# Optimization experiments

Hardware: AMD Instinct MI355X
Metric: run time of the kernel (lower is better)

## Reference

```python
import jax, jax.numpy as jnp
import numpy as np

B, S, D, H, KV = 2, 2048, 1024, 16, 64
NUM_BUCKETS, MAX_DIST = 32, 128
LN_EPS = 1e-6


def _relative_position_bucket(rel_pos, num_buckets=NUM_BUCKETS, max_distance=MAX_DIST):
    # bidirectional (encoder) T5 bucketing
    nb = num_buckets // 2
    rb = (rel_pos > 0).astype(jnp.int32) * nb
    rp = jnp.abs(rel_pos)
    max_exact = nb // 2
    is_small = rp < max_exact
    rp_f = jnp.maximum(rp, 1).astype(jnp.float32)
    large = max_exact + (
        jnp.log(rp_f / max_exact) / np.log(max_distance / max_exact) * (nb - max_exact)
    ).astype(jnp.int32)
    large = jnp.minimum(large, nb - 1)
    return rb + jnp.where(is_small, rp, large)


def _compute_bias(rel_emb, q_len, k_len):
    ctx = jnp.arange(q_len)[:, None]
    mem = jnp.arange(k_len)[None, :]
    buckets = _relative_position_bucket(mem - ctx)            # (q, k)
    bias = rel_emb[buckets]                                   # (q, k, H)
    return jnp.transpose(bias, (2, 0, 1))[None]               # (1, H, q, k)


def setup_inputs() -> dict:
    key = jax.random.key(0)
    ks = jax.random.split(key, 8)
    return {
        "hidden_states": jax.random.normal(ks[0], (B, S, D), jnp.float32),
        "attention_mask": jnp.zeros((B, 1, 1, S), jnp.float32),
        "delete_gate_mask": jax.random.normal(ks[1], (B, S, 1), jnp.float32),
        "wq": jax.random.normal(ks[2], (D, H * KV), jnp.float32) * 0.02,
        "wk": jax.random.normal(ks[3], (D, H * KV), jnp.float32) * 0.02,
        "wv": jax.random.normal(ks[4], (D, H * KV), jnp.float32) * 0.02,
        "wo": jax.random.normal(ks[5], (H * KV, D), jnp.float32) * 0.02,
        "rel_emb": jax.random.normal(ks[6], (NUM_BUCKETS, H), jnp.float32) * 0.5,
        "ln_weight": jnp.ones((D,), jnp.float32),
    }


def reference(hidden_states, attention_mask, delete_gate_mask, wq, wk, wv, wo, rel_emb, ln_weight):
    # T5LayerNorm: RMS norm, no mean subtraction, no bias
    var = jnp.mean(jnp.square(hidden_states), axis=-1, keepdims=True)
    normed = hidden_states * jax.lax.rsqrt(var + LN_EPS) * ln_weight

    # project and split heads: (B, H, S, KV). T5 does NOT scale by 1/sqrt(d).
    q = jnp.einsum('bsd,dhk->bhsk', normed, wq.reshape(D, H, KV))
    k = jnp.einsum('bsd,dhk->bhsk', normed, wk.reshape(D, H, KV))
    v = jnp.einsum('bsd,dhk->bhsk', normed, wv.reshape(D, H, KV))

    scores = jnp.einsum('bhqk,bhmk->bhqm', q, k)              # (B, H, S, S)

    position_bias = _compute_bias(rel_emb, S, S) + attention_mask  # (B, H, S, S) via broadcast
    scores = scores + position_bias
    # delete gate: (B, S, 1) -> additive over key axis
    scores = scores + delete_gate_mask[:, :, 0][:, None, None, :]

    attn = jax.nn.softmax(scores.astype(jnp.float32), axis=-1).astype(scores.dtype)
    ctx = jnp.einsum('bhqm,bhmk->bhqk', attn, v)              # (B, H, S, KV)
    ctx = jnp.transpose(ctx, (0, 2, 1, 3)).reshape(B, S, H * KV)
    attn_out = ctx @ wo                                       # (B, S, D)

    return hidden_states + attn_out
```

## Files before the change

### kernel.cpp

```cpp
#include <hip/hip_runtime.h>
#include <math.h>

#define SQ_LEN 2048
#define NB 2
#define DIM 1024
#define NH 16
#define BS (NB * SQ_LEN)

typedef __attribute__((ext_vector_type(8))) unsigned short ushort8;
typedef __attribute__((ext_vector_type(8))) __bf16 bf16x8;
typedef __attribute__((ext_vector_type(4))) float f32x4;

__device__ __forceinline__ unsigned short f2bfu(float x) {
    __bf16 h = (__bf16)x;
    return __builtin_bit_cast(unsigned short, h);
}
__device__ __forceinline__ bf16x8 ldb8(const unsigned short* p) {
    return __builtin_bit_cast(bf16x8, *(const ushort8*)p);
}
__device__ __forceinline__ void gl16(const unsigned short* g, unsigned short* l) {
    __builtin_amdgcn_global_load_lds(
        (const __attribute__((address_space(1))) unsigned int*)g,
        (__attribute__((address_space(3))) unsigned int*)l, 16, 0, 0);
}
__device__ __forceinline__ int pxor(int row) {
    return (((row & 7) ^ (((row >> 3) & 1) << 1)) << 3);
}
#define MFMA16(a, b, c) __builtin_amdgcn_mfma_f32_16x16x32_bf16(a, b, c, 0, 0, 0)
#define SM_SHIFT 16.0f

__global__ __launch_bounds__(256) void k_bias_table(const float* __restrict__ rel_emb,
                                                    float* __restrict__ table) {
    int i = blockIdx.x * 256 + threadIdx.x;
    int h = i >> 12;
    int idx = i & 4095;
    int rel = idx - 2048;
    int rb = (rel > 0) ? 16 : 0;
    int rp = rel < 0 ? -rel : rel;
    int v;
    if (rp < 8) {
        v = rp;
    } else {
        double lg = log((double)rp / 8.0) / log(16.0) * 8.0;
        int li = (int)lg;
        v = 8 + li;
        if (v > 15) v = 15;
    }
    table[i] = rel_emb[(rb + v) * NH + h] - SM_SHIFT;
}

__global__ __launch_bounds__(256) void k_kvbias(const float* __restrict__ am,
                                                const float* __restrict__ dg,
                                                float* __restrict__ kvb) {
    int i = blockIdx.x * 256 + threadIdx.x;
    kvb[i] = am[i] + dg[i];
}

__global__ __launch_bounds__(256) void k_wconv(const float* __restrict__ w0,
                                               const float* __restrict__ w1,
                                               const float* __restrict__ w2,
                                               const float* __restrict__ w3,
                                               unsigned short* __restrict__ wt) {
    int z = blockIdx.z;
    const float* w = (z == 0) ? w0 : (z == 1) ? w1 : (z == 2) ? w2 : w3;
    unsigned short* o = wt + (size_t)z * DIM * DIM;
    __shared__ float tile[64][68];
    int k0 = blockIdx.x * 64, n0 = blockIdx.y * 64;
    int t = threadIdx.x;
    {
        int r = t & 63, cs = (t >> 6) * 16;
#pragma unroll
        for (int u = 0; u < 4; ++u) {
            float4 v4 = *(const float4*)(w + (size_t)(k0 + r) * DIM + n0 + cs + 4 * u);
            *(float4*)&tile[r][cs + 4 * u] = v4;
        }
    }
    __syncthreads();
    {
        int n = t & 63, ks = (t >> 6) * 16;
        unsigned buf[8];
#pragma unroll
        for (int kk = 0; kk < 8; ++kk) {
            buf[kk] = (unsigned)f2bfu(tile[ks + 2 * kk][n]) |
                      ((unsigned)f2bfu(tile[ks + 2 * kk + 1][n]) << 16);
        }
        unsigned short* op = o + (size_t)(n0 + n) * DIM + k0 + ks;
        *(uint4*)op = make_uint4(buf[0], buf[1], buf[2], buf[3]);
        *(uint4*)(op + 8) = make_uint4(buf[4], buf[5], buf[6], buf[7]);
    }
}

__global__ __launch_bounds__(256) void k_rmsnorm(const float* __restrict__ x,
                                                 const float* __restrict__ w,
                                                 unsigned short* __restrict__ o) {
    int row = blockIdx.x;
    int t = threadIdx.x;
    float4 v = ((const float4*)(x + (size_t)row * DIM))[t];
    float ss = v.x * v.x + v.y * v.y + v.z * v.z + v.w * v.w;
#pragma unroll
    for (int m = 1; m < 64; m <<= 1) ss += __shfl_xor(ss, m);
    __shared__ float wsum[4];
    if ((t & 63) == 0) wsum[t >> 6] = ss;
    __syncthreads();
    float tot = wsum[0] + wsum[1] + wsum[2] + wsum[3];
    float r = rsqrtf(tot * (1.0f / DIM) + 1e-6f);
    float4 wt = ((const float4*)w)[t];
    uint2 pk;
    pk.x = (unsigned)f2bfu(v.x * r * wt.x) | ((unsigned)f2bfu(v.y * r * wt.y) << 16);
    pk.y = (unsigned)f2bfu(v.z * r * wt.z) | ((unsigned)f2bfu(v.w * r * wt.w) << 16);
    *(uint2*)(o + (size_t)row * DIM + t * 4) = pk;
}

__global__ __launch_bounds__(256) void k_gemm_qkv(const unsigned short* __restrict__ A,
                                                  const unsigned short* __restrict__ Wt,
                                                  unsigned short* __restrict__ Qo,
                                                  unsigned short* __restrict__ Ko,
                                                  unsigned short* __restrict__ Vto) {
    __shared__ unsigned short As[128 * 64];
    __shared__ unsigned short Bs[128 * 64];
    int m0 = blockIdx.x * 128;
    int mat = blockIdx.y >> 3;
    int n0 = (blockIdx.y & 7) * 128;
    const unsigned short* Bp = Wt + (size_t)mat * (DIM * DIM);
    int t = threadIdx.x;
    int w = t >> 6, l = t & 63;
    int wm = (w >> 1) * 64, wn = (w & 1) * 64;
    int g = l >> 4, n16 = l & 15;
    int c0 = (g ^ (n16 & 7)) * 8;
    int c1 = ((4 + g) ^ (n16 & 7)) * 8;
    f32x4 acc[4][4];
#pragma unroll
    for (int i = 0; i < 4; ++i)
#pragma unroll
        for (int j = 0; j < 4; ++j) acc[i][j] = 0.0f;

    for (int k0 = 0; k0 < DIM; k0 += 64) {
        __syncthreads();
#pragma unroll
        for (int u = 0; u < 4; ++u) {
            int ci = t + 256 * u;
            int row = ci >> 3;
            int sc = ((ci & 7) ^ (row & 7)) * 8;
            gl16(A + (size_t)(m0 + row) * DIM + k0 + sc, &As[ci * 8]);
            gl16(Bp + (size_t)(n0 + row) * DIM + k0 + sc, &Bs[ci * 8]);
        }
        __syncthreads();
        bf16x8 af[2][4], bf[2][4];
#pragma unroll
        for (int ks = 0; ks < 2; ++ks) {
            int cs = ks ? c1 : c0;
#pragma unroll
            for (int x = 0; x < 4; ++x) {
                af[ks][x] = ldb8(&As[(wm + x * 16 + n16) * 64 + cs]);
                bf[ks][x] = ldb8(&Bs[(wn + x * 16 + n16) * 64 + cs]);
            }
        }
#pragma unroll
        for (int ks = 0; ks < 2; ++ks)
#pragma unroll
            for (int mf = 0; mf < 4; ++mf)
#pragma unroll
                for (int nf = 0; nf < 4; ++nf)
                    acc[mf][nf] = MFMA16(af[ks][mf], bf[ks][nf], acc[mf][nf]);
    }
    if (mat < 2) {
        unsigned short* C = (mat == 0) ? Qo : Ko;
#pragma unroll
        for (int mf = 0; mf < 4; ++mf)
#pragma unroll
            for (int nf = 0; nf < 4; ++nf) {
                size_t base = (size_t)(m0 + wm + mf * 16 + 4 * g) * DIM + (n0 + wn + nf * 16 + n16);
#pragma unroll
                for (int r = 0; r < 4; ++r) C[base + (size_t)r * DIM] = f2bfu(acc[mf][nf][r]);
            }
    } else {
        int b = m0 >> 11;
        int sq = (m0 & 2047) + wm;
#pragma unroll
        for (int mf = 0; mf < 4; ++mf)
#pragma unroll
            for (int nf = 0; nf < 4; ++nf) {
                int n = n0 + wn + nf * 16 + n16;
                int s = sq + mf * 16 + 4 * g;
                uint2 pk;
                pk.x = (unsigned)f2bfu(acc[mf][nf][0]) | ((unsigned)f2bfu(acc[mf][nf][1]) << 16);
                pk.y = (unsigned)f2bfu(acc[mf][nf][2]) | ((unsigned)f2bfu(acc[mf][nf][3]) << 16);
                *(uint2*)(Vto + ((size_t)b << 21) + (size_t)n * SQ_LEN + s) = pk;
            }
    }
}

__global__ __launch_bounds__(256) void k_gemm_out(const unsigned short* __restrict__ A,
                                                  const unsigned short* __restrict__ Bt,
                                                  const float* __restrict__ resid,
                                                  float* __restrict__ Co) {
    __shared__ unsigned short As[128 * 64];
    __shared__ unsigned short Bs[128 * 64];
    int m0 = blockIdx.x * 128;
    int n0 = blockIdx.y * 128;
    int t = threadIdx.x;
    int w = t >> 6, l = t & 63;
    int wm = (w >> 1) * 64, wn = (w & 1) * 64;
    int g = l >> 4, n16 = l & 15;
    int c0 = (g ^ (n16 & 7)) * 8;
    int c1 = ((4 + g) ^ (n16 & 7)) * 8;
    f32x4 acc[4][4];
#pragma unroll
    for (int i = 0; i < 4; ++i)
#pragma unroll
        for (int j = 0; j < 4; ++j) acc[i][j] = 0.0f;

    for (int k0 = 0; k0 < DIM; k0 += 64) {
        __syncthreads();
#pragma unroll
        for (int u = 0; u < 4; ++u) {
            int ci = t + 256 * u;
            int row = ci >> 3;
            int sc = ((ci & 7) ^ (row & 7)) * 8;
            gl16(A + (size_t)(m0 + row) * DIM + k0 + sc, &As[ci * 8]);
            gl16(Bt + (size_t)(n0 + row) * DIM + k0 + sc, &Bs[ci * 8]);
        }
        __syncthreads();
        bf16x8 af[2][4], bf[2][4];
#pragma unroll
        for (int ks = 0; ks < 2; ++ks) {
            int cs = ks ? c1 : c0;
#pragma unroll
            for (int x = 0; x < 4; ++x) {
                af[ks][x] = ldb8(&As[(wm + x * 16 + n16) * 64 + cs]);
                bf[ks][x] = ldb8(&Bs[(wn + x * 16 + n16) * 64 + cs]);
            }
        }
#pragma unroll
        for (int ks = 0; ks < 2; ++ks)
#pragma unroll
            for (int mf = 0; mf < 4; ++mf)
#pragma unroll
                for (int nf = 0; nf < 4; ++nf)
                    acc[mf][nf] = MFMA16(af[ks][mf], bf[ks][nf], acc[mf][nf]);
    }
#pragma unroll
    for (int mf = 0; mf < 4; ++mf)
#pragma unroll
        for (int nf = 0; nf < 4; ++nf) {
            size_t base = (size_t)(m0 + wm + mf * 16 + 4 * g) * DIM + (n0 + wn + nf * 16 + n16);
#pragma unroll
            for (int r = 0; r < 4; ++r) {
                size_t off = base + (size_t)r * DIM;
                Co[off] = acc[mf][nf][r] + resid[off];
            }
        }
}

__global__ __launch_bounds__(256) void k_attn(const unsigned short* __restrict__ Q,
                                              const unsigned short* __restrict__ K,
                                              const unsigned short* __restrict__ Vt,
                                              const float* __restrict__ table,
                                              const float* __restrict__ kvb,
                                              unsigned short* __restrict__ ctx) {
    int qt = blockIdx.x;
    int bh = blockIdx.y;
    int b = bh >> 4, h = bh & 15;
    int qbase = qt * 128;

    __shared__ unsigned short Ks[64 * 64];
    __shared__ unsigned short Vs[64 * 64];
    __shared__ unsigned short Ps[4][32 * 64];
    __shared__ float tabR[4][200];

    int t = threadIdx.x, w = t >> 6, l = t & 63;
    int g = l >> 4, n16 = l & 15;
    int c0 = (g ^ (n16 & 7)) * 8;
    int c1 = ((4 + g) ^ (n16 & 7)) * 8;
    int pxr = pxor(n16);

    const unsigned short* qp = Q + (size_t)(b * SQ_LEN + qbase + 32 * w) * DIM + h * 64;
    const unsigned short* kp = K + (size_t)(b * SQ_LEN) * DIM + h * 64;
    const unsigned short* vp = Vt + ((size_t)b << 21) + (size_t)(h * 64) * SQ_LEN;
    const float* tabh = table + h * 4096;

    bf16x8 aq[2][2];
#pragma unroll
    for (int sub = 0; sub < 2; ++sub)
#pragma unroll
        for (int ks = 0; ks < 2; ++ks)
            aq[sub][ks] = ldb8(qp + (size_t)(sub * 16 + n16) * DIM + ks * 32 + g * 8);

    float sl[2][4] = {};
    f32x4 o[2][4];
#pragma unroll
    for (int sub = 0; sub < 2; ++sub)
#pragma unroll
        for (int f = 0; f < 4; ++f) o[sub][f] = 0.0f;

    int base_i[2];
#pragma unroll
    for (int sub = 0; sub < 2; ++sub)
        base_i[sub] = 130 - 32 * w + n16 - 16 * sub - 4 * g;
    int tb = 1918 - qbase;

    for (int kt = 0; kt < SQ_LEN / 64; ++kt) {
        __syncthreads();
        {
#pragma unroll
            for (int u = 0; u < 2; ++u) {
                int ci = t + 256 * u;
                int row = ci >> 3;
                int sc = ((ci & 7) ^ (row & 7)) * 8;
                gl16(kp + (size_t)(kt * 64 + row) * DIM + sc, &Ks[ci * 8]);
                gl16(vp + (size_t)row * SQ_LEN + kt * 64 + sc, &Vs[ci * 8]);
            }
        }
        {
#pragma unroll
            for (int u = 0; u < 4; ++u) {
                int e = t + 256 * u;
                int m = e >> 8, j = e & 255;
                if (j < 194) {
                    int gi = kt * 64 + tb + j + m;
                    gi = gi < 0 ? 0 : (gi > 4095 ? 4095 : gi);
                    tabR[m][j] = tabh[gi];
                }
            }
        }
        __syncthreads();

        const float* kvbp = kvb + b * SQ_LEN + kt * 64 + n16;
        f32x4 s4[2][4];
#pragma unroll
        for (int sub = 0; sub < 2; ++sub)
#pragma unroll
            for (int f = 0; f < 4; ++f) {
                int s = base_i[sub] + 16 * f - 3;
                int m = s & 3;
                f32x4 tv = *(const f32x4*)&tabR[m][s - m];
                float kb = kvbp[f * 16];
                f32x4 iv;
                iv[0] = tv[3] + kb; iv[1] = tv[2] + kb;
                iv[2] = tv[1] + kb; iv[3] = tv[0] + kb;
                s4[sub][f] = iv;
            }
#pragma unroll
        for (int ks = 0; ks < 2; ++ks) {
            int cs = ks ? c1 : c0;
#pragma unroll
            for (int f = 0; f < 4; ++f) {
                bf16x8 kf = ldb8(&Ks[(f * 16 + n16) * 64 + cs]);
#pragma unroll
                for (int sub = 0; sub < 2; ++sub)
                    s4[sub][f] = MFMA16(aq[sub][ks], kf, s4[sub][f]);
            }
        }
#pragma unroll
        for (int sub = 0; sub < 2; ++sub)
#pragma unroll
            for (int f = 0; f < 4; ++f) {
#pragma unroll
                for (int r = 0; r < 4; ++r) {
                    float p = __expf(s4[sub][f][r]);
                    sl[sub][r] += p;
                    int pr = sub * 16 + 4 * g + r;
                    Ps[w][pr * 64 + ((f * 16 + n16) ^ pxor(pr))] = f2bfu(p);
                }
            }
#pragma unroll
        for (int ks = 0; ks < 2; ++ks) {
            int cs = ks ? c1 : c0;
            int csp = ((ks ? (4 + g) : g) * 8) ^ pxr;
            bf16x8 ap[2];
#pragma unroll
            for (int sub = 0; sub < 2; ++sub)
                ap[sub] = ldb8(&Ps[w][(sub * 16 + n16) * 64 + csp]);
#pragma unroll
            for (int f = 0; f < 4; ++f) {
                bf16x8 vf = ldb8(&Vs[(f * 16 + n16) * 64 + cs]);
#pragma unroll
                for (int sub = 0; sub < 2; ++sub)
                    o[sub][f] = MFMA16(ap[sub], vf, o[sub][f]);
            }
        }
    }
    float inv[2][4];
#pragma unroll
    for (int sub = 0; sub < 2; ++sub)
#pragma unroll
        for (int r = 0; r < 4; ++r) {
            float s = sl[sub][r];
            s += __shfl_xor(s, 1);
            s += __shfl_xor(s, 2);
            s += __shfl_xor(s, 4);
            s += __shfl_xor(s, 8);
            inv[sub][r] = 1.0f / s;
        }
    unsigned short* cp = ctx + (size_t)(b * SQ_LEN + qbase + 32 * w) * DIM + h * 64;
#pragma unroll
    for (int sub = 0; sub < 2; ++sub)
#pragma unroll
        for (int f = 0; f < 4; ++f)
#pragma unroll
            for (int r = 0; r < 4; ++r)
                cp[(size_t)(sub * 16 + 4 * g + r) * DIM + f * 16 + n16] =
                    f2bfu(o[sub][f][r] * inv[sub][r]);
}

extern "C" void kernel_launch(void* const* d_in, const int* in_sizes, int n_in,
                              void* d_out, int out_size, void* d_ws, size_t ws_size,
                              hipStream_t stream) {
    const float* hidden = (const float*)d_in[0];
    const float* amask  = (const float*)d_in[1];
    const float* dg     = (const float*)d_in[2];
    const float* wq     = (const float*)d_in[3];
    const float* wk     = (const float*)d_in[4];
    const float* wv     = (const float*)d_in[5];
    const float* wo     = (const float*)d_in[6];
    const float* rel    = (const float*)d_in[7];
    const float* lnw    = (const float*)d_in[8];
    float* out = (float*)d_out;
    char* ws = (char*)d_ws;

    const size_t MB8 = (size_t)BS * DIM * 2;
    unsigned short* normed = (unsigned short*)(ws);
    unsigned short* qb     = (unsigned short*)(ws + MB8);
    unsigned short* kb     = (unsigned short*)(ws + 2 * MB8);
    unsigned short* vtb    = (unsigned short*)(ws + 3 * MB8);
    unsigned short* ctxb   = (unsigned short*)(ws + 4 * MB8);
    unsigned short* wt     = (unsigned short*)(ws + 5 * MB8);
    float* table           = (float*)(ws + 6 * MB8);
    float* kvb             = (float*)(ws + 6 * MB8 + NH * 4096 * 4);

    k_wconv<<<dim3(16, 16, 4), 256, 0, stream>>>(wq, wk, wv, wo, wt);
    k_bias_table<<<NH * 4096 / 256, 256, 0, stream>>>(rel, table);
    k_kvbias<<<BS / 256, 256, 0, stream>>>(amask, dg, kvb);
    k_rmsnorm<<<BS, 256, 0, stream>>>(hidden, lnw, normed);

    k_gemm_qkv<<<dim3(BS / 128, 24), 256, 0, stream>>>(normed, wt, qb, kb, vtb);
    k_attn<<<dim3(SQ_LEN / 128, NB * NH), 256, 0, stream>>>(qb, kb, vtb, table, kvb, ctxb);
    k_gemm_out<<<dim3(BS / 128, 8), 256, 0, stream>>>(ctxb, wt + 3 * (size_t)DIM * DIM,
                                                      hidden, out);
}
```

Before: 234.1 us.

## Use 8 waves per attention block, smaller out-GEMM tiles, merge prep kernels

The attention kernel now runs 512 threads per block, so each wave handles 16 query rows instead of 32. This halves per-wave register state and gives more waves to hide latency, at the cost of more K/V LDS reads per MFMA. The output GEMM moves from 128x128 to 64x64 tiles, giving four times as many blocks to fill the GPU but less data reuse per block. The bias-table and kv-bias kernels are merged into one launch to remove a kernel launch.

```diff
diff --git a/kernel.cpp b/kernel.cpp
--- a/kernel.cpp
+++ b/kernel.cpp
@@ -29,8 +29,11 @@
 #define MFMA16(a, b, c) __builtin_amdgcn_mfma_f32_16x16x32_bf16(a, b, c, 0, 0, 0)
 #define SM_SHIFT 16.0f
 
-__global__ __launch_bounds__(256) void k_bias_table(const float* __restrict__ rel_emb,
-                                                    float* __restrict__ table) {
+__global__ __launch_bounds__(256) void k_prep(const float* __restrict__ rel_emb,
+                                              const float* __restrict__ am,
+                                              const float* __restrict__ dg,
+                                              float* __restrict__ table,
+                                              float* __restrict__ kvb) {
     int i = blockIdx.x * 256 + threadIdx.x;
     int h = i >> 12;
     int idx = i & 4095;
@@ -47,13 +50,7 @@
         if (v > 15) v = 15;
     }
     table[i] = rel_emb[(rb + v) * NH + h] - SM_SHIFT;
-}
-
-__global__ __launch_bounds__(256) void k_kvbias(const float* __restrict__ am,
-                                                const float* __restrict__ dg,
-                                                float* __restrict__ kvb) {
-    int i = blockIdx.x * 256 + threadIdx.x;
-    kvb[i] = am[i] + dg[i];
+    if (i < BS) kvb[i] = am[i] + dg[i];
 }
 
 __global__ __launch_bounds__(256) void k_wconv(const float* __restrict__ w0,
@@ -194,26 +191,26 @@
                                                   const unsigned short* __restrict__ Bt,
                                                   const float* __restrict__ resid,
                                                   float* __restrict__ Co) {
-    __shared__ unsigned short As[128 * 64];
-    __shared__ unsigned short Bs[128 * 64];
-    int m0 = blockIdx.x * 128;
-    int n0 = blockIdx.y * 128;
+    __shared__ unsigned short As[64 * 64];
+    __shared__ unsigned short Bs[64 * 64];
+    int m0 = blockIdx.x * 64;
+    int n0 = blockIdx.y * 64;
     int t = threadIdx.x;
     int w = t >> 6, l = t & 63;
-    int wm = (w >> 1) * 64, wn = (w & 1) * 64;
+    int wm = (w >> 1) * 32, wn = (w & 1) * 32;
     int g = l >> 4, n16 = l & 15;
     int c0 = (g ^ (n16 & 7)) * 8;
     int c1 = ((4 + g) ^ (n16 & 7)) * 8;
-    f32x4 acc[4][4];
-#pragma unroll
-    for (int i = 0; i < 4; ++i)
-#pragma unroll
-        for (int j = 0; j < 4; ++j) acc[i][j] = 0.0f;
+    f32x4 acc[2][2];
+#pragma unroll
+    for (int i = 0; i < 2; ++i)
+#pragma unroll
+        for (int j = 0; j < 2; ++j) acc[i][j] = 0.0f;
 
     for (int k0 = 0; k0 < DIM; k0 += 64) {
         __syncthreads();
 #pragma unroll
-        for (int u = 0; u < 4; ++u) {
+        for (int u = 0; u < 2; ++u) {
             int ci = t + 256 * u;
             int row = ci >> 3;
             int sc = ((ci & 7) ^ (row & 7)) * 8;
@@ -221,12 +218,12 @@
             gl16(Bt + (size_t)(n0 + row) * DIM + k0 + sc, &Bs[ci * 8]);
         }
         __syncthreads();
-        bf16x8 af[2][4], bf[2][4];
+        bf16x8 af[2][2], bf[2][2];
 #pragma unroll
         for (int ks = 0; ks < 2; ++ks) {
             int cs = ks ? c1 : c0;
 #pragma unroll
-            for (int x = 0; x < 4; ++x) {
+            for (int x = 0; x < 2; ++x) {
                 af[ks][x] = ldb8(&As[(wm + x * 16 + n16) * 64 + cs]);
                 bf[ks][x] = ldb8(&Bs[(wn + x * 16 + n16) * 64 + cs]);
             }
@@ -234,15 +231,15 @@
 #pragma unroll
         for (int ks = 0; ks < 2; ++ks)
 #pragma unroll
-            for (int mf = 0; mf < 4; ++mf)
-#pragma unroll
-                for (int nf = 0; nf < 4; ++nf)
+            for (int mf = 0; mf < 2; ++mf)
+#pragma unroll
+                for (int nf = 0; nf < 2; ++nf)
                     acc[mf][nf] = MFMA16(af[ks][mf], bf[ks][nf], acc[mf][nf]);
     }
 #pragma unroll
-    for (int mf = 0; mf < 4; ++mf)
-#pragma unroll
-        for (int nf = 0; nf < 4; ++nf) {
+    for (int mf = 0; mf < 2; ++mf)
+#pragma unroll
+        for (int nf = 0; nf < 2; ++nf) {
             size_t base = (size_t)(m0 + wm + mf * 16 + 4 * g) * DIM + (n0 + wn + nf * 16 + n16);
 #pragma unroll
             for (int r = 0; r < 4; ++r) {
@@ -252,7 +249,7 @@
         }
 }
 
-__global__ __launch_bounds__(256) void k_attn(const unsigned short* __restrict__ Q,
+__global__ __launch_bounds__(512) void k_attn(const unsigned short* __restrict__ Q,
                                               const unsigned short* __restrict__ K,
                                               const unsigned short* __restrict__ Vt,
                                               const float* __restrict__ table,
@@ -265,7 +262,7 @@
 
     __shared__ unsigned short Ks[64 * 64];
     __shared__ unsigned short Vs[64 * 64];
-    __shared__ unsigned short Ps[4][32 * 64];
+    __shared__ unsigned short Ps[8][16 * 64];
     __shared__ float tabR[4][200];
 
     int t = threadIdx.x, w = t >> 6, l = t & 63;
@@ -274,49 +271,39 @@
     int c1 = ((4 + g) ^ (n16 & 7)) * 8;
     int pxr = pxor(n16);
 
-    const unsigned short* qp = Q + (size_t)(b * SQ_LEN + qbase + 32 * w) * DIM + h * 64;
+    const unsigned short* qp = Q + (size_t)(b * SQ_LEN + qbase + 16 * w) * DIM + h * 64;
     const unsigned short* kp = K + (size_t)(b * SQ_LEN) * DIM + h * 64;
     const unsigned short* vp = Vt + ((size_t)b << 21) + (size_t)(h * 64) * SQ_LEN;
     const float* tabh = table + h * 4096;
 
-    bf16x8 aq[2][2];
-#pragma unroll
-    for (int sub = 0; sub < 2; ++sub)
-#pragma unroll
-        for (int ks = 0; ks < 2; ++ks)
-            aq[sub][ks] = ldb8(qp + (size_t)(sub * 16 + n16) * DIM + ks * 32 + g * 8);
-
-    float sl[2][4] = {};
-    f32x4 o[2][4];
-#pragma unroll
-    for (int sub = 0; sub < 2; ++sub)
-#pragma unroll
-        for (int f = 0; f < 4; ++f) o[sub][f] = 0.0f;
-
-    int base_i[2];
-#pragma unroll
-    for (int sub = 0; sub < 2; ++sub)
-        base_i[sub] = 130 - 32 * w + n16 - 16 * sub - 4 * g;
+    bf16x8 aq[2];
+#pragma unroll
+    for (int ks = 0; ks < 2; ++ks)
+        aq[ks] = ldb8(qp + (size_t)n16 * DIM + ks * 32 + g * 8);
+
+    float sl[4] = {};
+    f32x4 o[4];
+#pragma unroll
+    for (int f = 0; f < 4; ++f) o[f] = 0.0f;
+
+    int base_i = 130 - 16 * w + n16 - 4 * g;
     int tb = 1918 - qbase;
 
     for (int kt = 0; kt < SQ_LEN / 64; ++kt) {
         __syncthreads();
         {
+            int ci = t;
+            int row = ci >> 3;
+            int sc = ((ci & 7) ^ (row & 7)) * 8;
+            gl16(kp + (size_t)(kt * 64 + row) * DIM + sc, &Ks[ci * 8]);
+            gl16(vp + (size_t)row * SQ_LEN + kt * 64 + sc, &Vs[ci * 8]);
+        }
+        {
 #pragma unroll
             for (int u = 0; u < 2; ++u) {
-                int ci = t + 256 * u;
-                int row = ci >> 3;
-                int sc = ((ci & 7) ^ (row & 7)) * 8;
-                gl16(kp + (size_t)(kt * 64 + row) * DIM + sc, &Ks[ci * 8]);
-                gl16(vp + (size_t)row * SQ_LEN + kt * 64 + sc, &Vs[ci * 8]);
-            }
-        }
-        {
-#pragma unroll
-            for (int u = 0; u < 4; ++u) {
-                int e = t + 256 * u;
+                int e = t + 512 * u;
                 int m = e >> 8, j = e & 255;
-                if (j < 194) {
+                if (j < 196) {
                     int gi = kt * 64 + tb + j + m;
                     gi = gi < 0 ? 0 : (gi > 4095 ? 4095 : gi);
                     tabR[m][j] = tabh[gi];
@@ -326,81 +313,65 @@
         __syncthreads();
 
         const float* kvbp = kvb + b * SQ_LEN + kt * 64 + n16;
-        f32x4 s4[2][4];
-#pragma unroll
-        for (int sub = 0; sub < 2; ++sub)
-#pragma unroll
-            for (int f = 0; f < 4; ++f) {
-                int s = base_i[sub] + 16 * f - 3;
-                int m = s & 3;
-                f32x4 tv = *(const f32x4*)&tabR[m][s - m];
-                float kb = kvbp[f * 16];
-                f32x4 iv;
-                iv[0] = tv[3] + kb; iv[1] = tv[2] + kb;
-                iv[2] = tv[1] + kb; iv[3] = tv[0] + kb;
-                s4[sub][f] = iv;
-            }
+        f32x4 s4[4];
+#pragma unroll
+        for (int f = 0; f < 4; ++f) {
+            int s = base_i + 16 * f - 3;
+            int m = s & 3;
+            f32x4 tv = *(const f32x4*)&tabR[m][s - m];
+            float kb = kvbp[f * 16];
+            f32x4 iv;
+            iv[0] = tv[3] + kb; iv[1] = tv[2] + kb;
+            iv[2] = tv[1] + kb; iv[3] = tv[0] + kb;
+            s4[f] = iv;
+        }
 #pragma unroll
         for (int ks = 0; ks < 2; ++ks) {
             int cs = ks ? c1 : c0;
 #pragma unroll
             for (int f = 0; f < 4; ++f) {
                 bf16x8 kf = ldb8(&Ks[(f * 16 + n16) * 64 + cs]);
-#pragma unroll
-                for (int sub = 0; sub < 2; ++sub)
-                    s4[sub][f] = MFMA16(aq[sub][ks], kf, s4[sub][f]);
-            }
-        }
-#pragma unroll
-        for (int sub = 0; sub < 2; ++sub)
-#pragma unroll
-            for (int f = 0; f < 4; ++f) {
-#pragma unroll
-                for (int r = 0; r < 4; ++r) {
-                    float p = __expf(s4[sub][f][r]);
-                    sl[sub][r] += p;
-                    int pr = sub * 16 + 4 * g + r;
-                    Ps[w][pr * 64 + ((f * 16 + n16) ^ pxor(pr))] = f2bfu(p);
-                }
-            }
+                s4[f] = MFMA16(aq[ks], kf, s4[f]);
+            }
+        }
+#pragma unroll
+        for (int f = 0; f < 4; ++f) {
+#pragma unroll
+            for (int r = 0; r < 4; ++r) {
+                float p = __expf(s4[f][r]);
+                sl[r] += p;
+                int pr = 4 * g + r;
+                Ps[w][pr * 64 + ((f * 16 + n16) ^ pxor(pr))] = f2bfu(p);
+            }
+        }
 #pragma unroll
         for (int ks = 0; ks < 2; ++ks) {
             int cs = ks ? c1 : c0;
             int csp = ((ks ? (4 + g) : g) * 8) ^ pxr;
-            bf16x8 ap[2];
-#pragma unroll
-            for (int sub = 0; sub < 2; ++sub)
-                ap[sub] = ldb8(&Ps[w][(sub * 16 + n16) * 64 + csp]);
+            bf16x8 ap = ldb8(&Ps[w][n16 * 64 + csp]);
 #pragma unroll
             for (int f = 0; f < 4; ++f) {
                 bf16x8 vf = ldb8(&Vs[(f * 16 + n16) * 64 + cs]);
-#pragma unroll
-                for (int sub = 0; sub < 2; ++sub)
-                    o[sub][f] = MFMA16(ap[sub], vf, o[sub][f]);
-            }
-        }
-    }
-    float inv[2][4];
-#pragma unroll
-    for (int sub = 0; sub < 2; ++sub)
-#pragma unroll
-        for (int r = 0; r < 4; ++r) {
-            float s = sl[sub][r];
-            s += __shfl_xor(s, 1);
-            s += __shfl_xor(s, 2);
-            s += __shfl_xor(s, 4);
-            s += __shfl_xor(s, 8);
-            inv[sub][r] = 1.0f / s;
-        }
-    unsigned short* cp = ctx + (size_t)(b * SQ_LEN + qbase + 32 * w) * DIM + h * 64;
-#pragma unroll
-    for (int sub = 0; sub < 2; ++sub)
-#pragma unroll
-        for (int f = 0; f < 4; ++f)
-#pragma unroll
-            for (int r = 0; r < 4; ++r)
-                cp[(size_t)(sub * 16 + 4 * g + r) * DIM + f * 16 + n16] =
-                    f2bfu(o[sub][f][r] * inv[sub][r]);
+                o[f] = MFMA16(ap, vf, o[f]);
+            }
+        }
+    }
+    float inv[4];
+#pragma unroll
+    for (int r = 0; r < 4; ++r) {
+        float s = sl[r];
+        s += __shfl_xor(s, 1);
+        s += __shfl_xor(s, 2);
+        s += __shfl_xor(s, 4);
+        s += __shfl_xor(s, 8);
+        inv[r] = 1.0f / s;
+    }
+    unsigned short* cp = ctx + (size_t)(b * SQ_LEN + qbase + 16 * w) * DIM + h * 64;
+#pragma unroll
+    for (int f = 0; f < 4; ++f)
+#pragma unroll
+        for (int r = 0; r < 4; ++r)
+            cp[(size_t)(4 * g + r) * DIM + f * 16 + n16] = f2bfu(o[f][r] * inv[r]);
 }
 
 extern "C" void kernel_launch(void* const* d_in, const int* in_sizes, int n_in,
@@ -429,12 +400,11 @@
     float* kvb             = (float*)(ws + 6 * MB8 + NH * 4096 * 4);
 
     k_wconv<<<dim3(16, 16, 4), 256, 0, stream>>>(wq, wk, wv, wo, wt);
-    k_bias_table<<<NH * 4096 / 256, 256, 0, stream>>>(rel, table);
-    k_kvbias<<<BS / 256, 256, 0, stream>>>(amask, dg, kvb);
+    k_prep<<<NH * 4096 / 256, 256, 0, stream>>>(rel, amask, dg, table, kvb);
     k_rmsnorm<<<BS, 256, 0, stream>>>(hidden, lnw, normed);
 
     k_gemm_qkv<<<dim3(BS / 128, 24), 256, 0, stream>>>(normed, wt, qb, kb, vtb);
-    k_attn<<<dim3(SQ_LEN / 128, NB * NH), 256, 0, stream>>>(qb, kb, vtb, table, kvb, ctxb);
-    k_gemm_out<<<dim3(BS / 128, 8), 256, 0, stream>>>(ctxb, wt + 3 * (size_t)DIM * DIM,
-                                                      hidden, out);
-}
+    k_attn<<<dim3(SQ_LEN / 128, NB * NH), 512, 0, stream>>>(qb, kb, vtb, table, kvb, ctxb);
+    k_gemm_out<<<dim3(BS / 64, DIM / 64), 256, 0, stream>>>(ctxb, wt + 3 * (size_t)DIM * DIM,
+                                                            hidden, out);
+}
```

Result: no change. 232.6 us (-0.6%).
